# Kernel optimization log

Measured on AMD Instinct MI355X. Metric: run time of the kernel, lower is better.

The kernel has to match this reference:

```python
import jax, jax.numpy as jnp
import numpy as np
from jax import lax

B, C, H, W = 32, 128, 56, 56
O, KS, K = 128, 3, 2
HIDDEN = 32  # int(in_planes * ratio)
TEMPERATURE = 31.0
STRIDE, PAD = 1, 1


def setup_inputs() -> dict:
    key = jax.random.key(0)
    ks = jax.random.split(key, 6)
    return {
        "x": jax.random.normal(ks[0], (B, C, H, W), jnp.float32),
        "common_weight": jax.random.normal(ks[1], (1, O, C, KS, KS), jnp.float32) * 0.05,
        "common_bias": jax.random.normal(ks[2], (1, O), jnp.float32) * 0.05,
        "dyn_weight": jax.random.normal(ks[3], (1, O, C, KS, KS), jnp.float32) * 0.05,
        "dyn_bias": jnp.zeros((1, O), jnp.float32),
        "fc1_w": jax.random.normal(ks[4], (HIDDEN, C), jnp.float32) * 0.1,
        "fc2_w": jax.random.normal(ks[5], (K, HIDDEN), jnp.float32) * 0.1,
    }


def reference(x, common_weight, common_bias, dyn_weight, dyn_bias, fc1_w, fc2_w):
    b, c, h, w = x.shape
    # attention2d: global avg pool -> 1x1 conv -> relu -> 1x1 conv -> softmax(./T)
    pooled = jnp.mean(x, axis=(2, 3))                       # [B, C]
    hid = jax.nn.relu(pooled @ fc1_w.T)                     # [B, hidden]
    logits = hid @ fc2_w.T                                  # [B, K]
    attn = jax.nn.softmax(logits / TEMPERATURE, axis=1)     # [B, K]

    # aggregate per-sample weights/biases from the K-bank
    weight_all = jnp.concatenate([common_weight, dyn_weight], axis=0)  # [K,O,C,k,k]
    agg_w = jnp.einsum('bk,kocij->bocij', attn, weight_all)            # [B,O,C,k,k]
    bias_all = jnp.concatenate([common_bias, dyn_bias], axis=0)       # [K,O]
    agg_b = attn @ bias_all                                            # [B,O]

    # per-sample conv via grouped conv with feature_group_count = batch
    x1 = x.reshape(1, b * c, h, w)
    w1 = agg_w.reshape(b * O, c, KS, KS)
    out = lax.conv_general_dilated(
        x1, w1,
        window_strides=(STRIDE, STRIDE),
        padding=((PAD, PAD), (PAD, PAD)),
        dimension_numbers=('NCHW', 'OIHW', 'NCHW'),
        feature_group_count=b,
    )  # [1, B*O, H', W']
    out = out.reshape(b, O, out.shape[-2], out.shape[-1])
    return out + agg_b[:, :, None, None]
```

## Files before the change

kernel.cpp:

```cpp
#include <hip/hip_runtime.h>


#define B_ 32
#define C_ 128
#define O_ 128
#define SP_ 3136

typedef __bf16  bf16x8 __attribute__((ext_vector_type(8)));
typedef short   short8 __attribute__((ext_vector_type(8)));
typedef float   f32x4  __attribute__((ext_vector_type(4)));

__device__ __forceinline__ short f2bf(float f) {
  unsigned u = __float_as_uint(f);
  u += 0x7fffu + ((u >> 16) & 1u);
  return (short)(u >> 16);
}
__device__ __forceinline__ float bf2f(short s) {
  return __uint_as_float(((unsigned)(unsigned short)s) << 16);
}

#define GLOAD_LDS16(gp, lp)                                                     \
  __builtin_amdgcn_global_load_lds(                                             \
      (const __attribute__((address_space(1))) unsigned int*)(gp),              \
      (__attribute__((address_space(3))) unsigned int*)(lp), 16, 0, 0)

#define WS_PARTIAL_F 0
#define WS_AGGB_F    229440
#define WS_ZERO_B    934144
#define WS_WB_B      935168
#define WS_XH_B      10372352

__global__ __launch_bounds__(256) void convert_k(const float* __restrict__ x,
                                                 char* __restrict__ wsbase) {
  const int h = blockIdx.x, b = blockIdx.y;
  const int tid = threadIdx.x;
  __shared__ short lc[C_ * 57];
  __shared__ float red[256];
  if (h == 0 && b == 0)
    ((int*)(wsbase + WS_ZERO_B))[tid] = 0;
  const float* xp = x + (size_t)b * C_ * SP_ + h * 56;
#pragma unroll
  for (int q = 0; q < 7; ++q) {
    int i = q * 256 + tid;
    int c = i / 14, w4 = (i - c * 14) * 4;
    float4 v = *reinterpret_cast<const float4*>(xp + (size_t)c * SP_ + w4);
    lc[c * 57 + w4 + 0] = f2bf(v.x);
    lc[c * 57 + w4 + 1] = f2bf(v.y);
    lc[c * 57 + w4 + 2] = f2bf(v.z);
    lc[c * 57 + w4 + 3] = f2bf(v.w);
  }
  __syncthreads();
  {
    const int c = tid & 127, half = tid >> 7;
    float s = 0.f;
#pragma unroll
    for (int w = half * 28; w < half * 28 + 28; ++w) s += bf2f(lc[c * 57 + w]);
    red[tid] = s;
  }
  __syncthreads();
  if (tid < C_) {
    float* partial = (float*)wsbase + WS_PARTIAL_F;
    partial[((size_t)b * 56 + h) * C_ + tid] = red[tid] + red[tid + 128];
  }
  short* xo = (short*)(wsbase + WS_XH_B) + ((size_t)b * 56 + h) * 56 * C_;
  for (int u = tid; u < 896; u += 256) {
    int w = u >> 4, cp = (u & 15) * 8;
    short8 v;
#pragma unroll
    for (int k = 0; k < 8; ++k) v[k] = lc[(cp + k) * 57 + w];
    *reinterpret_cast<short8*>(xo + w * C_ + cp) = v;
  }
}

__global__ __launch_bounds__(256) void wagg2_k(const float* __restrict__ w0,
                                               const float* __restrict__ w1,
                                               const float* __restrict__ fc1,
                                               const float* __restrict__ fc2,
                                               const float* __restrict__ cbias,
                                               const float* __restrict__ dbias,
                                               char* __restrict__ wsbase) {
  const int b = blockIdx.x >> 3, og = blockIdx.x & 7;
  const int o0 = og * 16;
  const int tid = threadIdx.x;
  const float* partial = (const float*)wsbase + WS_PARTIAL_F;
  __shared__ float red[256];
  __shared__ float pooled_s[C_];
  __shared__ float hid[32];
  __shared__ float lg[2];
  __shared__ float at[2];
  __shared__ short wl[9 * 16 * C_];

  {
    const int c = tid & 127, half = tid >> 7;
    float s = 0.f;
    for (int hh = half * 28; hh < half * 28 + 28; ++hh)
      s += partial[((size_t)b * 56 + hh) * C_ + c];
    red[tid] = s;
  }
  __syncthreads();
  if (tid < C_) pooled_s[tid] = (red[tid] + red[tid + 128]) * (1.f / 3136.f);
  __syncthreads();
  {
    const int hd = tid >> 3, part = tid & 7;
    const float4* fa = reinterpret_cast<const float4*>(fc1 + hd * C_ + part * 16);
    const float4* pa = reinterpret_cast<const float4*>(pooled_s + part * 16);
    float s = 0.f;
#pragma unroll
    for (int i = 0; i < 4; ++i) {
      float4 f = fa[i], p = pa[i];
      s += f.x * p.x + f.y * p.y + f.z * p.z + f.w * p.w;
    }
    red[tid] = s;
  }
  __syncthreads();
  if (tid < 32) {
    float v = 0.f;
#pragma unroll
    for (int j = 0; j < 8; ++j) v += red[tid * 8 + j];
    hid[tid] = fmaxf(v, 0.f);
  }
  __syncthreads();
  if (tid < 64) red[tid] = hid[tid & 31] * fc2[tid];
  __syncthreads();
  if (tid < 2) {
    float l = 0.f;
#pragma unroll
    for (int hh = 0; hh < 32; ++hh) l += red[tid * 32 + hh];
    lg[tid] = l * (1.f / 31.f);
  }
  __syncthreads();
  if (tid == 0) {
    float m = fmaxf(lg[0], lg[1]);
    float e0 = __expf(lg[0] - m), e1 = __expf(lg[1] - m);
    float inv = 1.f / (e0 + e1);
    at[0] = e0 * inv; at[1] = e1 * inv;
  }
  __syncthreads();
  const float a0 = at[0], a1 = at[1];
  if (og == 0 && tid < C_) {
    float* aggb = (float*)wsbase + WS_AGGB_F;
    aggb[b * O_ + tid] = a0 * cbias[tid] + a1 * dbias[tid];
  }
#pragma unroll
  for (int it = 0; it < 8; ++it) {
    int r = it * 256 + tid;
    int o = o0 + (r >> 7), c = r & 127;
    size_t base = ((size_t)o * C_ + c) * 9;
#pragma unroll
    for (int j = 0; j < 9; ++j) {
      float v = a0 * w0[base + j] + a1 * w1[base + j];
      wl[j * 2048 + r] = f2bf(v);
    }
  }
  __syncthreads();
  short* Wb = (short*)(wsbase + WS_WB_B);
#pragma unroll
  for (int it = 0; it < 9; ++it) {
    int u = it * 256 + tid;
    int ij = u >> 8, v = (u & 255) * 8;
    *reinterpret_cast<short8*>(Wb + (((size_t)b * 9 + ij) * O_ + o0) * C_ + v) =
        *reinterpret_cast<const short8*>(&wl[ij * 2048 + v]);
  }
}

#define BUNITS5 928
#define BBUF5 14848
#define AOFF5 29696
#define ABUF5 8192
__global__ __launch_bounds__(256) void conv5_k(const char* __restrict__ wsbase,
                                               float* __restrict__ out) {
  const int flat = blockIdx.x;
  const int swz = (flat & 7) * 112 + (flat >> 3);
  const int b = swz / 28, ht = swz - b * 28;
  const int h0 = ht * 2;
  const int tid = threadIdx.x;
  const int lane = tid & 63, wv = tid >> 6;
  const int obase = wv * 32;
  const int l15 = lane & 15, g = lane >> 4;
  const float* aggb = (const float*)wsbase + WS_AGGB_F;

  __shared__ __align__(16) char xs[AOFF5 + 2 * ABUF5];

  const char* gsrcB[4];
  bool gact[4];
#pragma unroll
  for (int it = 0; it < 4; ++it) {
    int u = it * 256 + tid;
    gact[it] = (u < BUNITS5);
    int uu = gact[it] ? u : 0;
    int pos = uu >> 2;
    int q = ((uu & 3) - (uu >> 4)) & 3;
    int r = pos / 58, wc = pos - r * 58;
    int h = h0 - 1 + r, w = wc - 1;
    bool val = (unsigned)h < 56u && (unsigned)w < 56u;
    gsrcB[it] = wsbase + (val ? (WS_XH_B + 2 * ((((b * 56 + h) * 56 + w) << 7) + q * 8))
                              : WS_ZERO_B);
  }
  const char* gsrcA[2];
#pragma unroll
  for (int it = 0; it < 2; ++it) {
    int u = it * 256 + tid;
    int o = u >> 2;
    int q = ((u & 3) - (u >> 4)) & 3;
    gsrcA[it] = wsbase + WS_WB_B + 2 * ((size_t)b * 147456 + o * C_ + q * 8);
  }
  int aoffR[2];
#pragma unroll
  for (int m = 0; m < 2; ++m) {
    int o = obase + m * 16 + l15;
    aoffR[m] = (o << 6) + (((g + (o >> 2)) & 3) << 4);
  }
  int ptile[7];
#pragma unroll
  for (int n = 0; n < 7; ++n) {
    int p = n * 16 + l15;
    int hl = p / 56, wl = p - hl * 56;
    ptile[n] = (hl + 1) * 58 + (wl + 1);
  }

  f32x4 acc[2][7];
#pragma unroll
  for (int m = 0; m < 2; ++m)
#pragma unroll
    for (int n = 0; n < 7; ++n) acc[m][n] = f32x4{0.f, 0.f, 0.f, 0.f};

#pragma unroll
  for (int it = 0; it < 4; ++it)
    if (gact[it]) GLOAD_LDS16(gsrcB[it], xs + it * 4096 + wv * 1024);
#pragma unroll
  for (int it = 0; it < 2; ++it)
    GLOAD_LDS16(gsrcA[it], xs + AOFF5 + it * 4096 + wv * 1024);
  asm volatile("s_waitcnt vmcnt(0)" ::: "memory");
  __builtin_amdgcn_s_barrier();

#pragma unroll
  for (int cc = 0; cc < 4; ++cc) {
#pragma unroll
    for (int ij = 0; ij < 9; ++ij) {
      const int s = cc * 9 + ij;
      const int apar = s & 1, bpar = cc & 1;
      if (s < 35) {
        const int s2 = s + 1, cc2 = s2 / 9, ij2 = s2 - cc2 * 9;
        const int adelta = 2 * (ij2 * 16384 + cc2 * 32);
#pragma unroll
        for (int it = 0; it < 2; ++it)
          GLOAD_LDS16(gsrcA[it] + adelta,
                      xs + AOFF5 + ((s2 & 1) ? ABUF5 : 0) + it * 4096 + wv * 1024);
      }
      if (ij == 0 && cc < 3) {
#pragma unroll
        for (int it = 0; it < 4; ++it)
          if (gact[it])
            GLOAD_LDS16(gsrcB[it] + (cc + 1) * 64,
                        xs + (bpar ? 0 : BBUF5) + it * 4096 + wv * 1024);
      }
      const char* abuf = xs + AOFF5 + (apar ? ABUF5 : 0);
      const char* bbuf = xs + (bpar ? BBUF5 : 0);
      bf16x8 af[2];
#pragma unroll
      for (int m = 0; m < 2; ++m)
        af[m] = *reinterpret_cast<const bf16x8*>(abuf + aoffR[m]);
      const int sh = (ij / 3 - 1) * 58 + (ij % 3 - 1);
      __builtin_amdgcn_s_setprio(1);
#pragma unroll
      for (int n = 0; n < 7; ++n) {
        int pp = ptile[n] + sh;
        int off = (pp << 6) + ((((pp >> 2) + g) & 3) << 4);
        bf16x8 bfr = *reinterpret_cast<const bf16x8*>(bbuf + off);
#pragma unroll
        for (int m = 0; m < 2; ++m)
          acc[m][n] = __builtin_amdgcn_mfma_f32_16x16x32_bf16(af[m], bfr, acc[m][n], 0, 0, 0);
      }
      __builtin_amdgcn_s_setprio(0);
      if (s < 35) {
        asm volatile("s_waitcnt vmcnt(0)" ::: "memory");
        __builtin_amdgcn_s_barrier();
      }
    }
  }

  const int r4 = g * 4;
#pragma unroll
  for (int m = 0; m < 2; ++m) {
    float bias[4];
#pragma unroll
    for (int j = 0; j < 4; ++j) bias[j] = aggb[b * O_ + obase + m * 16 + r4 + j];
#pragma unroll
    for (int n = 0; n < 7; ++n) {
      int p = n * 16 + l15;
      int h = h0 + p / 56, w = p % 56;
#pragma unroll
      for (int j = 0; j < 4; ++j) {
        int o = obase + m * 16 + r4 + j;
        out[((size_t)(b * O_ + o) * 56 + h) * 56 + w] = acc[m][n][j] + bias[j];
      }
    }
  }
}

extern "C" void kernel_launch(void* const* d_in, const int* in_sizes, int n_in,
                              void* d_out, int out_size, void* d_ws, size_t ws_size,
                              hipStream_t stream) {
  const float* x   = (const float*)d_in[0];
  const float* cw  = (const float*)d_in[1];
  const float* cb  = (const float*)d_in[2];
  const float* dw  = (const float*)d_in[3];
  const float* db  = (const float*)d_in[4];
  const float* fc1 = (const float*)d_in[5];
  const float* fc2 = (const float*)d_in[6];
  float* out = (float*)d_out;
  char* wsb  = (char*)d_ws;

  convert_k<<<dim3(56, B_), 256, 0, stream>>>(x, wsb);
  wagg2_k<<<256, 256, 0, stream>>>(cw, dw, fc1, fc2, cb, db, wsb);
  conv5_k<<<896, 256, 0, stream>>>(wsb, out);
}
```

Baseline: 157.4 us.

## Load weight fragments directly from global into registers, dropping LDS A staging

The weight aggregation kernel now writes weights in a layout tiled by channel chunk and tap, so each wave can read its MFMA A-fragments directly from global memory into registers. The conv kernel no longer stages weights through double-buffered LDS, which removes the per-tap barriers: synchronisation drops from 35 barriers to 3, one per channel chunk. LDS use shrinks to the input tile only, which may allow higher occupancy. In exchange, 18 bf16x8 fragments per chunk are held in registers, raising register pressure, and the global-load latency for those fragments is exposed at the start of each chunk.

```diff
diff --git a/kernel.cpp b/kernel.cpp
--- a/kernel.cpp
+++ b/kernel.cpp
@@ -157,17 +157,18 @@
 #pragma unroll
   for (int it = 0; it < 9; ++it) {
     int u = it * 256 + tid;
-    int ij = u >> 8, v = (u & 255) * 8;
-    *reinterpret_cast<short8*>(Wb + (((size_t)b * 9 + ij) * O_ + o0) * C_ + v) =
-        *reinterpret_cast<const short8*>(&wl[ij * 2048 + v]);
-  }
-}
-
-#define BUNITS5 928
-#define BBUF5 14848
-#define AOFF5 29696
-#define ABUF5 8192
-__global__ __launch_bounds__(256) void conv5_k(const char* __restrict__ wsbase,
+    int ij = u >> 8, r8 = (u & 255) * 8;
+    int o = o0 + (r8 >> 7), c = r8 & 127;
+    int cc = c >> 5, c32 = c & 31;
+    size_t idx = (size_t)b * 147456 + cc * 36864 + ij * 4096 + o * 32 + c32;
+    *reinterpret_cast<short8*>(Wb + idx) =
+        *reinterpret_cast<const short8*>(&wl[ij * 2048 + r8]);
+  }
+}
+
+#define BUNITS6 928
+#define BBUF6 14848
+__global__ __launch_bounds__(256) void conv6_k(const char* __restrict__ wsbase,
                                                float* __restrict__ out) {
   const int flat = blockIdx.x;
   const int swz = (flat & 7) * 112 + (flat >> 3);
@@ -179,14 +180,14 @@
   const int l15 = lane & 15, g = lane >> 4;
   const float* aggb = (const float*)wsbase + WS_AGGB_F;
 
-  __shared__ __align__(16) char xs[AOFF5 + 2 * ABUF5];
+  __shared__ __align__(16) char xs[2 * BBUF6];
 
   const char* gsrcB[4];
   bool gact[4];
 #pragma unroll
   for (int it = 0; it < 4; ++it) {
     int u = it * 256 + tid;
-    gact[it] = (u < BUNITS5);
+    gact[it] = (u < BUNITS6);
     int uu = gact[it] ? u : 0;
     int pos = uu >> 2;
     int q = ((uu & 3) - (uu >> 4)) & 3;
@@ -196,20 +197,11 @@
     gsrcB[it] = wsbase + (val ? (WS_XH_B + 2 * ((((b * 56 + h) * 56 + w) << 7) + q * 8))
                               : WS_ZERO_B);
   }
-  const char* gsrcA[2];
-#pragma unroll
-  for (int it = 0; it < 2; ++it) {
-    int u = it * 256 + tid;
-    int o = u >> 2;
-    int q = ((u & 3) - (u >> 4)) & 3;
-    gsrcA[it] = wsbase + WS_WB_B + 2 * ((size_t)b * 147456 + o * C_ + q * 8);
-  }
-  int aoffR[2];
-#pragma unroll
-  for (int m = 0; m < 2; ++m) {
-    int o = obase + m * 16 + l15;
-    aoffR[m] = (o << 6) + (((g + (o >> 2)) & 3) << 4);
-  }
+  const char* abase = wsbase + WS_WB_B + (size_t)b * 294912;
+  int aoffm[2];
+#pragma unroll
+  for (int m = 0; m < 2; ++m)
+    aoffm[m] = (obase + m * 16 + l15) * 64 + g * 16;
   int ptile[7];
 #pragma unroll
   for (int n = 0; n < 7; ++n) {
@@ -227,39 +219,29 @@
 #pragma unroll
   for (int it = 0; it < 4; ++it)
     if (gact[it]) GLOAD_LDS16(gsrcB[it], xs + it * 4096 + wv * 1024);
-#pragma unroll
-  for (int it = 0; it < 2; ++it)
-    GLOAD_LDS16(gsrcA[it], xs + AOFF5 + it * 4096 + wv * 1024);
   asm volatile("s_waitcnt vmcnt(0)" ::: "memory");
   __builtin_amdgcn_s_barrier();
 
 #pragma unroll
   for (int cc = 0; cc < 4; ++cc) {
+    bf16x8 af[9][2];
+#pragma unroll
+    for (int ij = 0; ij < 9; ++ij)
+#pragma unroll
+      for (int m = 0; m < 2; ++m)
+        af[ij][m] = *reinterpret_cast<const bf16x8*>(
+            abase + cc * 73728 + ij * 8192 + aoffm[m]);
+    const int bpar = cc & 1;
+    if (cc < 3) {
+#pragma unroll
+      for (int it = 0; it < 4; ++it)
+        if (gact[it])
+          GLOAD_LDS16(gsrcB[it] + (cc + 1) * 64,
+                      xs + (bpar ? 0 : BBUF6) + it * 4096 + wv * 1024);
+    }
+    const char* bbuf = xs + (bpar ? BBUF6 : 0);
 #pragma unroll
     for (int ij = 0; ij < 9; ++ij) {
-      const int s = cc * 9 + ij;
-      const int apar = s & 1, bpar = cc & 1;
-      if (s < 35) {
-        const int s2 = s + 1, cc2 = s2 / 9, ij2 = s2 - cc2 * 9;
-        const int adelta = 2 * (ij2 * 16384 + cc2 * 32);
-#pragma unroll
-        for (int it = 0; it < 2; ++it)
-          GLOAD_LDS16(gsrcA[it] + adelta,
-                      xs + AOFF5 + ((s2 & 1) ? ABUF5 : 0) + it * 4096 + wv * 1024);
-      }
-      if (ij == 0 && cc < 3) {
-#pragma unroll
-        for (int it = 0; it < 4; ++it)
-          if (gact[it])
-            GLOAD_LDS16(gsrcB[it] + (cc + 1) * 64,
-                        xs + (bpar ? 0 : BBUF5) + it * 4096 + wv * 1024);
-      }
-      const char* abuf = xs + AOFF5 + (apar ? ABUF5 : 0);
-      const char* bbuf = xs + (bpar ? BBUF5 : 0);
-      bf16x8 af[2];
-#pragma unroll
-      for (int m = 0; m < 2; ++m)
-        af[m] = *reinterpret_cast<const bf16x8*>(abuf + aoffR[m]);
       const int sh = (ij / 3 - 1) * 58 + (ij % 3 - 1);
       __builtin_amdgcn_s_setprio(1);
 #pragma unroll
@@ -269,13 +251,13 @@
         bf16x8 bfr = *reinterpret_cast<const bf16x8*>(bbuf + off);
 #pragma unroll
         for (int m = 0; m < 2; ++m)
-          acc[m][n] = __builtin_amdgcn_mfma_f32_16x16x32_bf16(af[m], bfr, acc[m][n], 0, 0, 0);
+          acc[m][n] = __builtin_amdgcn_mfma_f32_16x16x32_bf16(af[ij][m], bfr, acc[m][n], 0, 0, 0);
       }
       __builtin_amdgcn_s_setprio(0);
-      if (s < 35) {
-        asm volatile("s_waitcnt vmcnt(0)" ::: "memory");
-        __builtin_amdgcn_s_barrier();
-      }
+    }
+    if (cc < 3) {
+      asm volatile("s_waitcnt vmcnt(0)" ::: "memory");
+      __builtin_amdgcn_s_barrier();
     }
   }
 
@@ -313,5 +295,5 @@
 
   convert_k<<<dim3(56, B_), 256, 0, stream>>>(x, wsb);
   wagg2_k<<<256, 256, 0, stream>>>(cw, dw, fc1, fc2, cb, db, wsb);
-  conv5_k<<<896, 256, 0, stream>>>(wsb, out);
-}
+  conv6_k<<<896, 256, 0, stream>>>(wsb, out);
+}
```

Measured after the change: 173.1 us. 10.0% more time.
